# Optimization experiments

Measured on AMD Instinct MI355X. Metric: run time of the kernel, lower is better.

The kernel has to match this reference:

```python
import jax, jax.numpy as jnp
import numpy as np
import math

N_HIDDEN = 256
N_BLOCKS = 15
N_BINARY = 8
NODE_DIM = 16
EDGE_DIM = 4
N_NODES = 20000
N_EDGES = 100000


def setup_inputs() -> dict:
    key = jax.random.key(0)
    ks = iter(jax.random.split(key, 64))

    def lin(i, o):
        return (jax.random.normal(next(ks), (i, o), jnp.float32) / np.sqrt(i)).astype(jnp.float32)

    def lin_s(i, o):  # stacked over N_BLOCKS layers
        return (jax.random.normal(next(ks), (N_BLOCKS, i, o), jnp.float32) / np.sqrt(i)).astype(jnp.float32)

    inp = {
        "x": jax.random.uniform(next(ks), (N_NODES, NODE_DIM), jnp.float32),
        "edge_index": jax.random.randint(next(ks), (2, N_EDGES), 0, N_NODES, jnp.int32),
        "edge_attr": jax.random.uniform(next(ks), (N_EDGES, EDGE_DIM), jnp.float32),
        # conv1: in = NODE_DIM
        "Wq1": lin(NODE_DIM, N_HIDDEN), "bq1": jnp.zeros((N_HIDDEN,), jnp.float32),
        "Wk1": lin(NODE_DIM, N_HIDDEN), "bk1": jnp.zeros((N_HIDDEN,), jnp.float32),
        "Wv1": lin(NODE_DIM, N_HIDDEN), "bv1": jnp.zeros((N_HIDDEN,), jnp.float32),
        "We1": lin(EDGE_DIM, N_HIDDEN),  # lin_edge has no bias in PyG TransformerConv
        "Ws1": lin(NODE_DIM, N_HIDDEN), "bs1": jnp.zeros((N_HIDDEN,), jnp.float32),
        # 15 residual blocks: in = N_HIDDEN, stacked params
        "Wq": lin_s(N_HIDDEN, N_HIDDEN), "bq": jnp.zeros((N_BLOCKS, N_HIDDEN), jnp.float32),
        "Wk": lin_s(N_HIDDEN, N_HIDDEN), "bk": jnp.zeros((N_BLOCKS, N_HIDDEN), jnp.float32),
        "Wv": lin_s(N_HIDDEN, N_HIDDEN), "bv": jnp.zeros((N_BLOCKS, N_HIDDEN), jnp.float32),
        "We": lin_s(EDGE_DIM, N_HIDDEN),
        "Ws": lin_s(N_HIDDEN, N_HIDDEN), "bs": jnp.zeros((N_BLOCKS, N_HIDDEN), jnp.float32),
        # output head
        "Wl": lin(N_HIDDEN, N_BINARY), "bl": jnp.zeros((N_BINARY,), jnp.float32),
        "scale": jnp.asarray([2.0 ** i for i in range(N_BINARY)], jnp.float32),
    }
    return inp


def _tconv(h, ea_emb_src_params, src, dst, n):
    """PyG TransformerConv (heads=1) with edge features."""
    wq, bq, wk, bk, wv, bv, we, ws, bs, ea = ea_emb_src_params
    q = h @ wq + bq          # [N, C]
    k = h @ wk + bk
    v = h @ wv + bv
    e = ea @ we              # [E, C] edge embedding
    ke = k[src] + e          # [E, C]
    alpha = jnp.sum(q[dst] * ke, axis=-1) / math.sqrt(N_HIDDEN)  # [E]
    m = jax.ops.segment_max(alpha, dst, num_segments=n)
    a = jnp.exp(alpha - m[dst])
    s = jax.ops.segment_sum(a, dst, num_segments=n)
    attn = a / (s[dst] + 1e-16)
    out = jax.ops.segment_sum(attn[:, None] * (v[src] + e), dst, num_segments=n)
    return out + h @ ws + bs  # root_weight skip


def reference(x, edge_index, edge_attr,
              Wq1, bq1, Wk1, bk1, Wv1, bv1, We1, Ws1, bs1,
              Wq, bq, Wk, bk, Wv, bv, We, Ws, bs,
              Wl, bl, scale):
    n = x.shape[0]
    src, dst = edge_index[0], edge_index[1]
    h = jnp.log(x + 1.0)
    ea = jnp.log(edge_attr + 1.0)
    h = _tconv(h, (Wq1, bq1, Wk1, bk1, Wv1, bv1, We1, Ws1, bs1, ea), src, dst, n)

    def block(carry, p):
        wq, bq_, wk, bk_, wv, bv_, we, ws, bs_ = p
        std = jax.lax.stop_gradient(jnp.std(carry, axis=-1, ddof=1, keepdims=True))
        h2 = jax.nn.relu(carry / std)
        y = _tconv(h2, (wq, bq_, wk, bk_, wv, bv_, we, ws, bs_, ea), src, dst, n)
        return carry + y, None

    h, _ = jax.lax.scan(block, h, (Wq, bq, Wk, bk, Wv, bv, We, Ws, bs))
    h = h / math.sqrt(N_BLOCKS)
    h = h @ Wl + bl
    return jnp.sum(h * scale, axis=-1, keepdims=True)
```

## Files before the change

### kernel.cpp

```cpp
#include <hip/hip_runtime.h>
#include <math.h>

typedef short bf16x8 __attribute__((ext_vector_type(8)));
typedef float f32x4 __attribute__((ext_vector_type(4)));
typedef _Float16 h16x8 __attribute__((ext_vector_type(8)));
typedef _Float16 h16x4 __attribute__((ext_vector_type(4)));
typedef _Float16 h16x2 __attribute__((ext_vector_type(2)));

static __device__ __forceinline__ float wred_sum(float v){
  #pragma unroll
  for (int o = 32; o > 0; o >>= 1) v += __shfl_xor(v, o, 64);
  return v;
}

static __device__ __forceinline__ unsigned short f2bf(float x){
  union { float f; unsigned int u; } c; c.f = x;
  unsigned int u = c.u;
  return (unsigned short)((u + 0x7FFFu + ((u >> 16) & 1u)) >> 16);
}

__global__ void prep_kernel(const float* __restrict__ x, const float* __restrict__ ea_in,
                            float* __restrict__ hx, float* __restrict__ ea,
                            int nx, int ne){
  int i = blockIdx.x * 256 + threadIdx.x;
  if (i < nx) hx[i] = logf(x[i] + 1.f);
  if (i < ne) ea[i] = logf(ea_in[i] + 1.f);
}

__global__ void zero_kernel(int* __restrict__ c, int n){
  int i = blockIdx.x * 256 + threadIdx.x;
  if (i < n) c[i] = 0;
}

__global__ void hist_kernel(const int* __restrict__ dst, int* __restrict__ counts, int E){
  int i = blockIdx.x * 256 + threadIdx.x;
  if (i < E) atomicAdd(&counts[dst[i]], 1);
}

__global__ __launch_bounds__(1024) void scan_kernel(const int* __restrict__ counts,
                                                    int* __restrict__ row_ptr,
                                                    int* __restrict__ cursor, int N){
  __shared__ int woff[16];
  __shared__ int carry_s;
  int t = threadIdx.x, lane = t & 63, wid = t >> 6;
  if (t == 0) carry_s = 0;
  __syncthreads();
  for (int base = 0; base < N; base += 1024){
    int i = base + t;
    int v = (i < N) ? counts[i] : 0;
    int incl = v;
    #pragma unroll
    for (int o = 1; o < 64; o <<= 1){
      int tmp = __shfl_up(incl, o, 64);
      if (lane >= o) incl += tmp;
    }
    if (lane == 63) woff[wid] = incl;
    __syncthreads();
    if (t < 16){
      int w = woff[t];
      int inc2 = w;
      #pragma unroll
      for (int o = 1; o < 16; o <<= 1){
        int tmp = __shfl_up(inc2, o, 16);
        if (t >= o) inc2 += tmp;
      }
      woff[t] = inc2 - w;
    }
    __syncthreads();
    int ex = carry_s + woff[wid] + incl - v;
    if (i < N){ row_ptr[i] = ex; cursor[i] = ex; }
    __syncthreads();
    if (t == 1023) carry_s = ex + v;
    __syncthreads();
  }
  if (t == 0) row_ptr[N] = carry_s;
}

__global__ void scatter_kernel(const int* __restrict__ src, const int* __restrict__ dst,
                               const float* __restrict__ ea,
                               int* __restrict__ cursor,
                               int* __restrict__ src_csr, float* __restrict__ ea_csr, int E){
  int i = blockIdx.x * 256 + threadIdx.x;
  if (i < E){
    int p = atomicAdd(&cursor[dst[i]], 1);
    src_csr[p] = src[i];
    *(float4*)&ea_csr[(size_t)p * 4] = *(const float4*)&ea[(size_t)i * 4];
  }
}

__global__ void wlscale_kernel(const float* __restrict__ Wl, const float* __restrict__ bl,
                               const float* __restrict__ scale, float* __restrict__ wlsc){
  int c = threadIdx.x;
  float s = 0.f;
  #pragma unroll
  for (int j = 0; j < 8; j++) s += Wl[c * 8 + j] * scale[j];
  wlsc[c] = s;
  if (c == 0){
    float b = 0.f;
    #pragma unroll
    for (int j = 0; j < 8; j++) b += bl[j] * scale[j];
    wlsc[256] = b;
  }
}

__global__ __launch_bounds__(256) void pack_w_kernel(
    const float* __restrict__ Wq, const float* __restrict__ Wk,
    const float* __restrict__ Wv, const float* __restrict__ Ws,
    unsigned short* __restrict__ Wp)
{
  __shared__ float t[32][33];
  int l   = blockIdx.z;
  int k0  = blockIdx.x * 32;
  int n0g = blockIdx.y * 32;
  int w   = n0g >> 8;
  int n0  = n0g & 255;
  const float* W = ((w == 0) ? Wq : (w == 1) ? Wk : (w == 2) ? Wv : Ws) + (size_t)l * 65536;
  int rr = threadIdx.x >> 3;
  int cc = (threadIdx.x & 7) * 4;
  float4 vv = *(const float4*)&W[(size_t)(k0 + rr) * 256 + n0 + cc];
  t[rr][cc + 0] = vv.x; t[rr][cc + 1] = vv.y; t[rr][cc + 2] = vv.z; t[rr][cc + 3] = vv.w;
  __syncthreads();
  ushort4 o;
  o.x = f2bf(t[cc + 0][rr]);
  o.y = f2bf(t[cc + 1][rr]);
  o.z = f2bf(t[cc + 2][rr]);
  o.w = f2bf(t[cc + 3][rr]);
  *(ushort4*)&Wp[(size_t)l * 262144 + (size_t)(n0g + rr) * 256 + k0 + cc] = o;
}

__global__ void pack_b_kernel(const float* __restrict__ bq, const float* __restrict__ bk,
                              const float* __restrict__ bv, const float* __restrict__ bs,
                              float* __restrict__ bp){
  int i = blockIdx.x * 256 + threadIdx.x;
  if (i < 15 * 256){
    int l = i >> 8, n = i & 255;
    bp[l * 1024 + 0   + n] = bq[i];
    bp[l * 1024 + 256 + n] = bk[i];
    bp[l * 1024 + 512 + n] = bv[i];
    bp[l * 1024 + 768 + n] = bs[i];
  }
}

__global__ __launch_bounds__(256) void pack_wqe_kernel(
    const float* __restrict__ Wq, const float* __restrict__ We,
    const float* __restrict__ bq, float* __restrict__ Wqe, float* __restrict__ bqe)
{
  __shared__ float We_s[1024];
  int l = blockIdx.x;
  for (int i = threadIdx.x; i < 1024; i += 256) We_s[i] = We[(size_t)l * 1024 + i];
  __syncthreads();
  int k = threadIdx.x;
  const float* wrow = Wq + (size_t)l * 65536 + (size_t)k * 256;
  float s0 = 0.f, s1 = 0.f, s2 = 0.f, s3 = 0.f;
  for (int c = 0; c < 256; c++){
    float wv = wrow[c];
    s0 += wv * We_s[c];
    s1 += wv * We_s[256 + c];
    s2 += wv * We_s[512 + c];
    s3 += wv * We_s[768 + c];
  }
  float4 o; o.x = s0; o.y = s1; o.z = s2; o.w = s3;
  *(float4*)&Wqe[((size_t)l * 256 + k) * 4] = o;
  if (k < 4){
    float b = 0.f;
    for (int c = 0; c < 256; c++) b += bq[l * 256 + c] * We_s[k * 256 + c];
    bqe[l * 4 + k] = b;
  }
}

__global__ __launch_bounds__(256) void qwe1_kernel(const _Float16* __restrict__ qkvh,
                                                   const float* __restrict__ We1,
                                                   float* __restrict__ qwe, int N){
  __shared__ float We_s[1024];
  for (int i = threadIdx.x; i < 1024; i += 256) We_s[i] = We1[i];
  __syncthreads();
  int wid = threadIdx.x >> 6, lane = threadIdx.x & 63;
  int n = blockIdx.x * 4 + wid;
  if (n >= N) return;
  int c0 = lane * 4;
  h16x4 qr = *(const h16x4*)&qkvh[(size_t)n * 768 + c0];
  float q0 = (float)qr[0], q1 = (float)qr[1], q2 = (float)qr[2], q3 = (float)qr[3];
  float4 o;
  #pragma unroll
  for (int j = 0; j < 4; j++){
    float s = q0 * We_s[j * 256 + c0] + q1 * We_s[j * 256 + c0 + 1]
            + q2 * We_s[j * 256 + c0 + 2] + q3 * We_s[j * 256 + c0 + 3];
    s = wred_sum(s);
    if (j == 0) o.x = s; else if (j == 1) o.y = s; else if (j == 2) o.z = s; else o.w = s;
  }
  if (lane == 0) *(float4*)&qwe[(size_t)n * 4] = o;
}

__global__ __launch_bounds__(256) void gemm1_kernel(
    const float* __restrict__ A,
    const float* __restrict__ W0, const float* __restrict__ W1,
    const float* __restrict__ W2, const float* __restrict__ W3,
    const float* __restrict__ B0, const float* __restrict__ B1,
    const float* __restrict__ B2, const float* __restrict__ B3,
    _Float16* __restrict__ qkvh, _Float16* __restrict__ slh, int N)
{
  __shared__ float As[64][16];
  int nb = blockIdx.x * 64;
  {
    int row = nb + (threadIdx.x >> 2);
    int qq = (threadIdx.x & 3) * 4;
    float4 a = make_float4(0.f, 0.f, 0.f, 0.f);
    if (row < N) a = *(const float4*)&A[row * 16 + qq];
    *(float4*)&As[threadIdx.x >> 2][qq] = a;
  }
  __syncthreads();
  int col = threadIdx.x;
  #pragma unroll
  for (int w = 0; w < 4; w++){
    const float* W  = (w == 0) ? W0 : (w == 1) ? W1 : (w == 2) ? W2 : W3;
    const float* Bi = (w == 0) ? B0 : (w == 1) ? B1 : (w == 2) ? B2 : B3;
    float wr[16];
    #pragma unroll
    for (int kk = 0; kk < 16; kk++) wr[kk] = W[kk * 256 + col];
    float bias = Bi[col];
    for (int r = 0; r < 64; r++){
      int row = nb + r;
      if (row >= N) break;
      float acc = bias;
      #pragma unroll
      for (int kk = 0; kk < 16; kk++) acc += As[r][kk] * wr[kk];
      if (w < 3) qkvh[(size_t)row * 768 + w * 256 + col] = (_Float16)acc;
      else       slh[(size_t)row * 256 + col] = (_Float16)acc;
    }
  }
}

__global__ __launch_bounds__(256, 3) void gemm_mfma_kernel(
    const unsigned short* __restrict__ A,
    const unsigned short* __restrict__ Wp,
    const float* __restrict__ bp,
    _Float16* __restrict__ qkvh,
    _Float16* __restrict__ slh,
    int M)
{
  __shared__ unsigned short lds[2 * 128 * 64];
  unsigned short* ldsA = lds;
  unsigned short* ldsB = lds + 128 * 64;
  const int tid  = threadIdx.x;
  const int wave = tid >> 6, lane = tid & 63;
  const int wm = wave >> 1, wn = wave & 1;
  const int rt  = (int)gridDim.x;
  const int lin = (int)blockIdx.x + rt * (int)blockIdx.y;
  const int gt  = (lin & 7) * rt + (lin >> 3);
  const int m0 = (gt >> 3) * 128;
  const int n0 = (gt & 7) * 128;

  f32x4 acc[4][4] = {};

  const int srow  = lane >> 3;
  const int sc16  = lane & 7;
  const int skgrp = sc16 ^ (srow & 7);

  for (int k0 = 0; k0 < 256; k0 += 64){
    #pragma unroll
    for (int it = 0; it < 4; ++it){
      int lrow = wave * 32 + it * 8;
      const unsigned short* gA = A + (size_t)(m0 + lrow + srow) * 256 + k0 + skgrp * 8;
      __builtin_amdgcn_global_load_lds((const __attribute__((address_space(1))) unsigned int*)gA,
          (__attribute__((address_space(3))) unsigned int*)(ldsA + lrow * 64), 16, 0, 0);
      const unsigned short* gB = Wp + (size_t)(n0 + lrow + srow) * 256 + k0 + skgrp * 8;
      __builtin_amdgcn_global_load_lds((const __attribute__((address_space(1))) unsigned int*)gB,
          (__attribute__((address_space(3))) unsigned int*)(ldsB + lrow * 64), 16, 0, 0);
    }
    __syncthreads();

    bf16x8 af[4][2], bfr[4][2];
    #pragma unroll
    for (int mb = 0; mb < 4; ++mb){
      int r = wm * 64 + mb * 16 + (lane & 15);
      #pragma unroll
      for (int ks = 0; ks < 2; ++ks){
        int kg = ks * 4 + (lane >> 4);
        af[mb][ks] = *(const bf16x8*)&ldsA[r * 64 + ((kg ^ (r & 7)) * 8)];
      }
    }
    #pragma unroll
    for (int nb = 0; nb < 4; ++nb){
      int r = wn * 64 + nb * 16 + (lane & 15);
      #pragma unroll
      for (int ks = 0; ks < 2; ++ks){
        int kg = ks * 4 + (lane >> 4);
        bfr[nb][ks] = *(const bf16x8*)&ldsB[r * 64 + ((kg ^ (r & 7)) * 8)];
      }
    }
    #pragma unroll
    for (int mb = 0; mb < 4; ++mb){
      #pragma unroll
      for (int nb = 0; nb < 4; ++nb){
        acc[mb][nb] = __builtin_amdgcn_mfma_f32_16x16x32_bf16(af[mb][0], bfr[nb][0], acc[mb][nb], 0, 0, 0);
        acc[mb][nb] = __builtin_amdgcn_mfma_f32_16x16x32_bf16(af[mb][1], bfr[nb][1], acc[mb][nb], 0, 0, 0);
      }
    }
    __syncthreads();
  }

  _Float16* lt = (_Float16*)lds;
  #pragma unroll
  for (int nb = 0; nb < 4; ++nb){
    int col = wn * 64 + nb * 16 + (lane & 15);
    float bias = bp[n0 + col];
    #pragma unroll
    for (int mb = 0; mb < 4; ++mb){
      #pragma unroll
      for (int r4 = 0; r4 < 4; ++r4){
        int row = wm * 64 + mb * 16 + (lane >> 4) * 4 + r4;
        lt[row * 128 + (col ^ (((row >> 2) & 3) << 4))] = (_Float16)(acc[mb][nb][r4] + bias);
      }
    }
  }
  __syncthreads();
  int tr = tid >> 4;
  int tc = (tid & 15) * 8;
  if (n0 < 768){
    #pragma unroll
    for (int it = 0; it < 8; ++it){
      int row = tr + it * 16;
      int grow = m0 + row;
      if (grow < M){
        h16x8 v8 = *(const h16x8*)&lt[row * 128 + (tc ^ (((row >> 2) & 3) << 4))];
        *(h16x8*)&qkvh[(size_t)grow * 768 + n0 + tc] = v8;
      }
    }
  } else {
    #pragma unroll
    for (int it = 0; it < 8; ++it){
      int row = tr + it * 16;
      int grow = m0 + row;
      if (grow < M){
        h16x8 v8 = *(const h16x8*)&lt[row * 128 + (tc ^ (((row >> 2) & 3) << 4))];
        *(h16x8*)&slh[(size_t)grow * 256 + (n0 - 768) + tc] = v8;
      }
    }
  }
}

__global__ __launch_bounds__(256) void agg_kernel(
    const _Float16* __restrict__ qkvh,
    const _Float16* __restrict__ slh,
    const float* __restrict__ qwe,
    const float* __restrict__ ea_csr,
    const int* __restrict__ src_csr,
    const float* __restrict__ We,
    const float* __restrict__ Wqe_next,
    const float* __restrict__ bqe_next,
    const int* __restrict__ row_ptr,
    const float* __restrict__ h_in, float* __restrict__ h_out,
    unsigned short* __restrict__ h2b, float* __restrict__ qwe_out,
    const float* __restrict__ wlsc, float* __restrict__ out,
    int RESID, int LAST, int N)
{
  int wid = threadIdx.x >> 6, lane = threadIdx.x & 63;
  int c0 = lane * 4;
  int glane = lane >> 3;
  int slane = lane & 7;
  union hu { h16x8 v; h16x2 p[4]; };
  int stride = (int)gridDim.x * 4;

  for (int n = blockIdx.x * 4 + wid; n < N; n += stride){
    int e0 = row_ptr[n], e1 = row_ptr[n + 1];
    float4 qwe4 = *(const float4*)&qwe[(size_t)n * 4];
    h16x4 slv4 = *(const h16x4*)&slh[(size_t)n * 256 + c0];
    float4 hp = make_float4(0.f, 0.f, 0.f, 0.f);
    if (RESID) hp = *(const float4*)&h_in[(size_t)n * 256 + c0];
    const _Float16* qrow = qkvh + (size_t)n * 768 + slane * 32;
    hu qf[4];
    #pragma unroll
    for (int u = 0; u < 4; ++u) qf[u].v = *(const h16x8*)(qrow + u * 8);

    float m = -INFINITY, ssum = 0.f;
    float a0 = 0.f, a1 = 0.f, a2 = 0.f, a3 = 0.f;
    float ec0 = 0.f, ec1 = 0.f, ec2 = 0.f, ec3 = 0.f;

    for (int base = e0; base < e1; base += 8){
      int cnt = min(8, e1 - base);
      int eg = base + ((glane < cnt) ? glane : (cnt - 1));
      int sg = src_csr[eg];
      int sj[8];
      #pragma unroll
      for (int j = 0; j < 8; ++j) sj[j] = __shfl(sg, j << 3, 64);
      float4 eag = *(const float4*)&ea_csr[(size_t)eg * 4];
      const _Float16* krow = qkvh + (size_t)sg * 768 + 256 + slane * 32;
      float dot = 0.f;
      #pragma unroll
      for (int u = 0; u < 4; ++u){
        hu kf;
        kf.v = *(const h16x8*)(krow + u * 8);
        #pragma unroll
        for (int pp = 0; pp < 4; ++pp){
#if __has_builtin(__builtin_amdgcn_fdot2)
          dot = __builtin_amdgcn_fdot2(qf[u].p[pp], kf.p[pp], dot, false);
#else
          dot += (float)qf[u].p[pp][0] * (float)kf.p[pp][0] + (float)qf[u].p[pp][1] * (float)kf.p[pp][1];
#endif
        }
      }
      #pragma unroll
      for (int o = 1; o < 8; o <<= 1) dot += __shfl_xor(dot, o, 64);
      float alpha_g = (dot + qwe4.x * eag.x + qwe4.y * eag.y + qwe4.z * eag.z + qwe4.w * eag.w) * 0.0625f;
      float aj[8];
      #pragma unroll
      for (int j = 0; j < 8; ++j){
        aj[j] = __shfl(alpha_g, j << 3, 64);
        if (j >= cnt) aj[j] = -INFINITY;
      }
      float mc = fmaxf(fmaxf(fmaxf(aj[0], aj[1]), fmaxf(aj[2], aj[3])),
                       fmaxf(fmaxf(aj[4], aj[5]), fmaxf(aj[6], aj[7])));
      float mn = fmaxf(m, mc);
      float corr = expf(m - mn);
      float wj[8];
      float wtot = 0.f;
      #pragma unroll
      for (int j = 0; j < 8; ++j){
        wj[j] = (j < cnt) ? expf(aj[j] - mn) : 0.f;
        wtot += wj[j];
      }
      ssum = ssum * corr + wtot;
      a0 *= corr; a1 *= corr; a2 *= corr; a3 *= corr;
      ec0 *= corr; ec1 *= corr; ec2 *= corr; ec3 *= corr;
      m = mn;
      #pragma unroll
      for (int j = 0; j < 8; ++j){
        if (j < cnt){
          h16x4 vr = *(const h16x4*)&qkvh[(size_t)sj[j] * 768 + 512 + c0];
          float4 er = *(const float4*)&ea_csr[(size_t)(base + j) * 4];
          a0 += wj[j] * (float)vr[0];
          a1 += wj[j] * (float)vr[1];
          a2 += wj[j] * (float)vr[2];
          a3 += wj[j] * (float)vr[3];
          ec0 += wj[j] * er.x;
          ec1 += wj[j] * er.y;
          ec2 += wj[j] * er.z;
          ec3 += wj[j] * er.w;
        }
      }
    }

    float inv = 1.f / (ssum + 1e-16f);
    float4 W0 = *(const float4*)&We[0 * 256 + c0];
    float4 W1 = *(const float4*)&We[1 * 256 + c0];
    float4 W2 = *(const float4*)&We[2 * 256 + c0];
    float4 W3 = *(const float4*)&We[3 * 256 + c0];
    float emb0 = ec0 * W0.x + ec1 * W1.x + ec2 * W2.x + ec3 * W3.x;
    float emb1 = ec0 * W0.y + ec1 * W1.y + ec2 * W2.y + ec3 * W3.y;
    float emb2 = ec0 * W0.z + ec1 * W1.z + ec2 * W2.z + ec3 * W3.z;
    float emb3 = ec0 * W0.w + ec1 * W1.w + ec2 * W2.w + ec3 * W3.w;
    float y0 = (a0 + emb0) * inv + (float)slv4[0];
    float y1 = (a1 + emb1) * inv + (float)slv4[1];
    float y2 = (a2 + emb2) * inv + (float)slv4[2];
    float y3 = (a3 + emb3) * inv + (float)slv4[3];
    float o0 = hp.x + y0, o1 = hp.y + y1, o2 = hp.z + y2, o3 = hp.w + y3;
    if (LAST){
      float4 wv = *(const float4*)&wlsc[c0];
      float pp = o0 * wv.x + o1 * wv.y + o2 * wv.z + o3 * wv.w;
      pp = wred_sum(pp);
      if (lane == 0) out[n] = pp * (1.f / sqrtf(15.f)) + wlsc[256];
      continue;
    }
    float4 ho; ho.x = o0; ho.y = o1; ho.z = o2; ho.w = o3;
    *(float4*)&h_out[(size_t)n * 256 + c0] = ho;
    float mean = wred_sum(o0 + o1 + o2 + o3) * (1.f / 256.f);
    float d0 = o0 - mean, d1 = o1 - mean, d2 = o2 - mean, d3 = o3 - mean;
    float var = wred_sum(d0 * d0 + d1 * d1 + d2 * d2 + d3 * d3) * (1.f / 255.f);
    float invstd = 1.f / sqrtf(var);
    float t0 = fmaxf(o0 * invstd, 0.f);
    float t1 = fmaxf(o1 * invstd, 0.f);
    float t2 = fmaxf(o2 * invstd, 0.f);
    float t3 = fmaxf(o3 * invstd, 0.f);
    ushort4 hb;
    hb.x = f2bf(t0); hb.y = f2bf(t1); hb.z = f2bf(t2); hb.w = f2bf(t3);
    *(ushort4*)&h2b[(size_t)n * 256 + c0] = hb;
    if (Wqe_next){
      float4 g0 = *(const float4*)&Wqe_next[(c0 + 0) * 4];
      float4 g1 = *(const float4*)&Wqe_next[(c0 + 1) * 4];
      float4 g2 = *(const float4*)&Wqe_next[(c0 + 2) * 4];
      float4 g3 = *(const float4*)&Wqe_next[(c0 + 3) * 4];
      float s0 = t0 * g0.x + t1 * g1.x + t2 * g2.x + t3 * g3.x;
      float s1 = t0 * g0.y + t1 * g1.y + t2 * g2.y + t3 * g3.y;
      float s2 = t0 * g0.z + t1 * g1.z + t2 * g2.z + t3 * g3.z;
      float s3 = t0 * g0.w + t1 * g1.w + t2 * g2.w + t3 * g3.w;
      s0 = wred_sum(s0); s1 = wred_sum(s1); s2 = wred_sum(s2); s3 = wred_sum(s3);
      if (lane == 0){
        float4 bq4 = *(const float4*)bqe_next;
        float4 o; o.x = s0 + bq4.x; o.y = s1 + bq4.y; o.z = s2 + bq4.z; o.w = s3 + bq4.w;
        *(float4*)&qwe_out[(size_t)n * 4] = o;
      }
    }
  }
}

extern "C" void kernel_launch(void* const* d_in, const int* in_sizes, int n_in,
                              void* d_out, int out_size, void* d_ws, size_t ws_size,
                              hipStream_t stream)
{
  const float* x     = (const float*)d_in[0];
  const int*   eidx  = (const int*)d_in[1];
  const float* Wq1 = (const float*)d_in[3];  const float* bq1 = (const float*)d_in[4];
  const float* Wk1 = (const float*)d_in[5];  const float* bk1 = (const float*)d_in[6];
  const float* Wv1 = (const float*)d_in[7];  const float* bv1 = (const float*)d_in[8];
  const float* We1 = (const float*)d_in[9];
  const float* Ws1 = (const float*)d_in[10]; const float* bs1 = (const float*)d_in[11];
  const float* Wq = (const float*)d_in[12];  const float* bq = (const float*)d_in[13];
  const float* Wk = (const float*)d_in[14];  const float* bk = (const float*)d_in[15];
  const float* Wv = (const float*)d_in[16];  const float* bv = (const float*)d_in[17];
  const float* We = (const float*)d_in[18];
  const float* Ws = (const float*)d_in[19];  const float* bs = (const float*)d_in[20];
  const float* Wl = (const float*)d_in[21];  const float* bl = (const float*)d_in[22];
  const float* scale = (const float*)d_in[23];
  (void)n_in; (void)ws_size;

  int N = in_sizes[0] / 16;
  int E = in_sizes[2] / 4;
  int Mpad = (N + 127) & ~127;
  float* out = (float*)d_out;
  (void)out_size;

  char* p = (char*)d_ws;
  auto alloc = [&](size_t bytes) -> char* {
    char* r = p; p += (bytes + 255) & ~(size_t)255; return r;
  };
  float* hx   = (float*)alloc((size_t)N * 16 * 4);
  float* ea   = (float*)alloc((size_t)E * 4 * 4);
  float* h    = (float*)alloc((size_t)N * 256 * 4);
  unsigned short* h2b = (unsigned short*)alloc((size_t)Mpad * 256 * 2);
  _Float16* qkvh = (_Float16*)alloc((size_t)N * 768 * 2);
  _Float16* slh  = (_Float16*)alloc((size_t)N * 256 * 2);
  float* qwe  = (float*)alloc((size_t)N * 4 * 4);
  float* ea_csr = (float*)alloc((size_t)E * 4 * 4);
  int* src_csr  = (int*)alloc((size_t)E * 4);
  unsigned short* Wp  = (unsigned short*)alloc((size_t)15 * 1024 * 256 * 2);
  float* bp   = (float*)alloc((size_t)15 * 1024 * 4);
  float* Wqe  = (float*)alloc((size_t)15 * 256 * 4 * 4);
  float* bqe  = (float*)alloc((size_t)15 * 4 * 4);
  float* wlsc = (float*)alloc(257 * 4);
  int* counts  = (int*)alloc((size_t)N * 4);
  int* cursor  = (int*)alloc((size_t)N * 4);
  int* row_ptr = (int*)alloc(((size_t)N + 1) * 4);

  const int* srcp = eidx;
  const int* dstp = eidx + E;

  int nx = N * 16, ne = E * 4;
  int big = nx > ne ? nx : ne;

  zero_kernel<<<(N + 255) / 256, 256, 0, stream>>>(counts, N);
  prep_kernel<<<(big + 255) / 256, 256, 0, stream>>>(x, (const float*)d_in[2], hx, ea, nx, ne);
  hist_kernel<<<(E + 255) / 256, 256, 0, stream>>>(dstp, counts, E);
  scan_kernel<<<1, 1024, 0, stream>>>(counts, row_ptr, cursor, N);
  scatter_kernel<<<(E + 255) / 256, 256, 0, stream>>>(srcp, dstp, ea, cursor,
                                                      src_csr, ea_csr, E);
  wlscale_kernel<<<1, 256, 0, stream>>>(Wl, bl, scale, wlsc);
  pack_w_kernel<<<dim3(8, 32, 15), 256, 0, stream>>>(Wq, Wk, Wv, Ws, Wp);
  pack_b_kernel<<<15, 256, 0, stream>>>(bq, bk, bv, bs, bp);
  pack_wqe_kernel<<<15, 256, 0, stream>>>(Wq, We, bq, Wqe, bqe);

  int agg_blocks = 1280;

  gemm1_kernel<<<(N + 63) / 64, 256, 0, stream>>>(hx, Wq1, Wk1, Wv1, Ws1,
                                                  bq1, bk1, bv1, bs1, qkvh, slh, N);
  qwe1_kernel<<<(N + 3) / 4, 256, 0, stream>>>(qkvh, We1, qwe, N);
  agg_kernel<<<agg_blocks, 256, 0, stream>>>(qkvh, slh, qwe, ea_csr, src_csr, We1,
                                             Wqe, bqe, row_ptr,
                                             h, h, h2b, qwe, wlsc, out, 0, 0, N);

  for (int l = 0; l < 15; l++){
    gemm_mfma_kernel<<<dim3(Mpad / 128, 8), 256, 0, stream>>>(
        h2b, Wp + (size_t)l * 262144, bp + (size_t)l * 1024, qkvh, slh, N);
    int last = (l == 14);
    const float* wqe_n = (l < 14) ? (Wqe + (size_t)(l + 1) * 1024) : nullptr;
    const float* bqe_n = (l < 14) ? (bqe + (size_t)(l + 1) * 4) : nullptr;
    agg_kernel<<<agg_blocks, 256, 0, stream>>>(qkvh, slh, qwe, ea_csr, src_csr,
                                               We + (size_t)l * 1024,
                                               wqe_n, bqe_n, row_ptr,
                                               h, h, h2b, qwe, wlsc, out, 1, last, N);
  }
}
```

Baseline: 1.165 ms.

## Process two nodes per wavefront in aggregation and store residual in fp16

The aggregation kernel now assigns one node per half-wavefront (32 lanes, 8 channels each) instead of one node per full wavefront, and launches one block per 8 nodes instead of a grid-stride loop. The residual state h is stored as fp16 instead of fp32, which halves its read and write traffic. This aims to raise memory-level parallelism and cut bytes moved in the gather-heavy aggregation. The cost is lane divergence when the two nodes in a wavefront have different degrees, since both halves run the larger trip count. The fp16 residual accumulated over 15 blocks also loses precision.

```diff
diff --git a/kernel.cpp b/kernel.cpp
--- a/kernel.cpp
+++ b/kernel.cpp
@@ -10,6 +10,12 @@
 static __device__ __forceinline__ float wred_sum(float v){
   #pragma unroll
   for (int o = 32; o > 0; o >>= 1) v += __shfl_xor(v, o, 64);
+  return v;
+}
+
+static __device__ __forceinline__ float hred_sum(float v){
+  #pragma unroll
+  for (int o = 16; o > 0; o >>= 1) v += __shfl_xor(v, o, 64);
   return v;
 }
 
@@ -349,146 +355,169 @@
     const float* __restrict__ Wqe_next,
     const float* __restrict__ bqe_next,
     const int* __restrict__ row_ptr,
-    const float* __restrict__ h_in, float* __restrict__ h_out,
+    const _Float16* __restrict__ h_in, _Float16* __restrict__ h_out,
     unsigned short* __restrict__ h2b, float* __restrict__ qwe_out,
     const float* __restrict__ wlsc, float* __restrict__ out,
-    int RESID, int LAST, int N)
+    int RESID, int LAST, int N, int E)
 {
   int wid = threadIdx.x >> 6, lane = threadIdx.x & 63;
-  int c0 = lane * 4;
-  int glane = lane >> 3;
-  int slane = lane & 7;
+  int half = lane >> 5, hl = lane & 31;
+  int n = blockIdx.x * 8 + wid * 2 + half;
+  bool valid = (n < N);
+  int nn = valid ? n : (N - 1);
+  int c0 = hl * 8;
+  int glane = hl >> 2;
+  int slane = hl & 3;
   union hu { h16x8 v; h16x2 p[4]; };
-  int stride = (int)gridDim.x * 4;
-
-  for (int n = blockIdx.x * 4 + wid; n < N; n += stride){
-    int e0 = row_ptr[n], e1 = row_ptr[n + 1];
-    float4 qwe4 = *(const float4*)&qwe[(size_t)n * 4];
-    h16x4 slv4 = *(const h16x4*)&slh[(size_t)n * 256 + c0];
-    float4 hp = make_float4(0.f, 0.f, 0.f, 0.f);
-    if (RESID) hp = *(const float4*)&h_in[(size_t)n * 256 + c0];
-    const _Float16* qrow = qkvh + (size_t)n * 768 + slane * 32;
-    hu qf[4];
-    #pragma unroll
-    for (int u = 0; u < 4; ++u) qf[u].v = *(const h16x8*)(qrow + u * 8);
-
-    float m = -INFINITY, ssum = 0.f;
-    float a0 = 0.f, a1 = 0.f, a2 = 0.f, a3 = 0.f;
-    float ec0 = 0.f, ec1 = 0.f, ec2 = 0.f, ec3 = 0.f;
-
-    for (int base = e0; base < e1; base += 8){
-      int cnt = min(8, e1 - base);
-      int eg = base + ((glane < cnt) ? glane : (cnt - 1));
-      int sg = src_csr[eg];
-      int sj[8];
+
+  int e0 = row_ptr[nn], e1 = row_ptr[nn + 1];
+  float4 qwe4 = *(const float4*)&qwe[(size_t)nn * 4];
+  h16x8 slv = *(const h16x8*)&slh[(size_t)nn * 256 + c0];
+  h16x8 hpv = {};
+  if (RESID) hpv = *(const h16x8*)&h_in[(size_t)nn * 256 + c0];
+  const _Float16* qrow = qkvh + (size_t)nn * 768 + slane * 64;
+  hu qf[8];
+  #pragma unroll
+  for (int u = 0; u < 8; ++u) qf[u].v = *(const h16x8*)(qrow + u * 8);
+
+  float m = -INFINITY, ssum = 0.f;
+  float a[8] = {};
+  float ec[4] = {};
+
+  int nch = (e1 - e0 + 7) >> 3;
+  int nco = __shfl_xor(nch, 32, 64);
+  int ntrip = nch > nco ? nch : nco;
+
+  for (int it = 0; it < ntrip; ++it){
+    int base = e0 + it * 8;
+    int cnt = e1 - base; if (cnt > 8) cnt = 8;
+    int off = (cnt > 0) ? ((glane < cnt) ? glane : cnt - 1) : 0;
+    int eg = base + off;
+    if (eg >= E) eg = E - 1;
+    int sg = src_csr[eg];
+    int sj[8];
+    #pragma unroll
+    for (int j = 0; j < 8; ++j) sj[j] = __shfl(sg, (half << 5) + (j << 2), 64);
+    float4 eag = *(const float4*)&ea_csr[(size_t)eg * 4];
+    const _Float16* krow = qkvh + (size_t)sg * 768 + 256 + slane * 64;
+    float dot = 0.f;
+    #pragma unroll
+    for (int u = 0; u < 8; ++u){
+      hu kf;
+      kf.v = *(const h16x8*)(krow + u * 8);
       #pragma unroll
-      for (int j = 0; j < 8; ++j) sj[j] = __shfl(sg, j << 3, 64);
-      float4 eag = *(const float4*)&ea_csr[(size_t)eg * 4];
-      const _Float16* krow = qkvh + (size_t)sg * 768 + 256 + slane * 32;
-      float dot = 0.f;
-      #pragma unroll
-      for (int u = 0; u < 4; ++u){
-        hu kf;
-        kf.v = *(const h16x8*)(krow + u * 8);
+      for (int pp = 0; pp < 4; ++pp){
+#if __has_builtin(__builtin_amdgcn_fdot2)
+        dot = __builtin_amdgcn_fdot2(qf[u].p[pp], kf.p[pp], dot, false);
+#else
+        dot += (float)qf[u].p[pp][0] * (float)kf.p[pp][0] + (float)qf[u].p[pp][1] * (float)kf.p[pp][1];
+#endif
+      }
+    }
+    dot += __shfl_xor(dot, 1, 64);
+    dot += __shfl_xor(dot, 2, 64);
+    float alpha_g = (dot + qwe4.x * eag.x + qwe4.y * eag.y + qwe4.z * eag.z + qwe4.w * eag.w) * 0.0625f;
+    float aj[8];
+    #pragma unroll
+    for (int j = 0; j < 8; ++j){
+      aj[j] = __shfl(alpha_g, (half << 5) + (j << 2), 64);
+      if (j >= cnt) aj[j] = -INFINITY;
+    }
+    float mc = fmaxf(fmaxf(fmaxf(aj[0], aj[1]), fmaxf(aj[2], aj[3])),
+                     fmaxf(fmaxf(aj[4], aj[5]), fmaxf(aj[6], aj[7])));
+    float mn = fmaxf(m, mc);
+    float corr = (mn > -INFINITY) ? expf(m - mn) : 0.f;
+    float wj[8];
+    float wtot = 0.f;
+    #pragma unroll
+    for (int j = 0; j < 8; ++j){
+      wj[j] = (j < cnt) ? expf(aj[j] - mn) : 0.f;
+      wtot += wj[j];
+    }
+    ssum = ssum * corr + wtot;
+    #pragma unroll
+    for (int i = 0; i < 8; ++i) a[i] *= corr;
+    #pragma unroll
+    for (int i = 0; i < 4; ++i) ec[i] *= corr;
+    m = mn;
+    #pragma unroll
+    for (int j = 0; j < 8; ++j){
+      if (j < cnt){
+        h16x8 vr = *(const h16x8*)&qkvh[(size_t)sj[j] * 768 + 512 + c0];
+        float4 er = *(const float4*)&ea_csr[(size_t)(base + j) * 4];
         #pragma unroll
-        for (int pp = 0; pp < 4; ++pp){
-#if __has_builtin(__builtin_amdgcn_fdot2)
-          dot = __builtin_amdgcn_fdot2(qf[u].p[pp], kf.p[pp], dot, false);
-#else
-          dot += (float)qf[u].p[pp][0] * (float)kf.p[pp][0] + (float)qf[u].p[pp][1] * (float)kf.p[pp][1];
-#endif
-        }
-      }
-      #pragma unroll
-      for (int o = 1; o < 8; o <<= 1) dot += __shfl_xor(dot, o, 64);
-      float alpha_g = (dot + qwe4.x * eag.x + qwe4.y * eag.y + qwe4.z * eag.z + qwe4.w * eag.w) * 0.0625f;
-      float aj[8];
-      #pragma unroll
-      for (int j = 0; j < 8; ++j){
-        aj[j] = __shfl(alpha_g, j << 3, 64);
-        if (j >= cnt) aj[j] = -INFINITY;
-      }
-      float mc = fmaxf(fmaxf(fmaxf(aj[0], aj[1]), fmaxf(aj[2], aj[3])),
-                       fmaxf(fmaxf(aj[4], aj[5]), fmaxf(aj[6], aj[7])));
-      float mn = fmaxf(m, mc);
-      float corr = expf(m - mn);
-      float wj[8];
-      float wtot = 0.f;
-      #pragma unroll
-      for (int j = 0; j < 8; ++j){
-        wj[j] = (j < cnt) ? expf(aj[j] - mn) : 0.f;
-        wtot += wj[j];
-      }
-      ssum = ssum * corr + wtot;
-      a0 *= corr; a1 *= corr; a2 *= corr; a3 *= corr;
-      ec0 *= corr; ec1 *= corr; ec2 *= corr; ec3 *= corr;
-      m = mn;
-      #pragma unroll
-      for (int j = 0; j < 8; ++j){
-        if (j < cnt){
-          h16x4 vr = *(const h16x4*)&qkvh[(size_t)sj[j] * 768 + 512 + c0];
-          float4 er = *(const float4*)&ea_csr[(size_t)(base + j) * 4];
-          a0 += wj[j] * (float)vr[0];
-          a1 += wj[j] * (float)vr[1];
-          a2 += wj[j] * (float)vr[2];
-          a3 += wj[j] * (float)vr[3];
-          ec0 += wj[j] * er.x;
-          ec1 += wj[j] * er.y;
-          ec2 += wj[j] * er.z;
-          ec3 += wj[j] * er.w;
-        }
-      }
-    }
-
-    float inv = 1.f / (ssum + 1e-16f);
-    float4 W0 = *(const float4*)&We[0 * 256 + c0];
-    float4 W1 = *(const float4*)&We[1 * 256 + c0];
-    float4 W2 = *(const float4*)&We[2 * 256 + c0];
-    float4 W3 = *(const float4*)&We[3 * 256 + c0];
-    float emb0 = ec0 * W0.x + ec1 * W1.x + ec2 * W2.x + ec3 * W3.x;
-    float emb1 = ec0 * W0.y + ec1 * W1.y + ec2 * W2.y + ec3 * W3.y;
-    float emb2 = ec0 * W0.z + ec1 * W1.z + ec2 * W2.z + ec3 * W3.z;
-    float emb3 = ec0 * W0.w + ec1 * W1.w + ec2 * W2.w + ec3 * W3.w;
-    float y0 = (a0 + emb0) * inv + (float)slv4[0];
-    float y1 = (a1 + emb1) * inv + (float)slv4[1];
-    float y2 = (a2 + emb2) * inv + (float)slv4[2];
-    float y3 = (a3 + emb3) * inv + (float)slv4[3];
-    float o0 = hp.x + y0, o1 = hp.y + y1, o2 = hp.z + y2, o3 = hp.w + y3;
-    if (LAST){
-      float4 wv = *(const float4*)&wlsc[c0];
-      float pp = o0 * wv.x + o1 * wv.y + o2 * wv.z + o3 * wv.w;
-      pp = wred_sum(pp);
-      if (lane == 0) out[n] = pp * (1.f / sqrtf(15.f)) + wlsc[256];
-      continue;
-    }
-    float4 ho; ho.x = o0; ho.y = o1; ho.z = o2; ho.w = o3;
-    *(float4*)&h_out[(size_t)n * 256 + c0] = ho;
-    float mean = wred_sum(o0 + o1 + o2 + o3) * (1.f / 256.f);
-    float d0 = o0 - mean, d1 = o1 - mean, d2 = o2 - mean, d3 = o3 - mean;
-    float var = wred_sum(d0 * d0 + d1 * d1 + d2 * d2 + d3 * d3) * (1.f / 255.f);
-    float invstd = 1.f / sqrtf(var);
-    float t0 = fmaxf(o0 * invstd, 0.f);
-    float t1 = fmaxf(o1 * invstd, 0.f);
-    float t2 = fmaxf(o2 * invstd, 0.f);
-    float t3 = fmaxf(o3 * invstd, 0.f);
-    ushort4 hb;
-    hb.x = f2bf(t0); hb.y = f2bf(t1); hb.z = f2bf(t2); hb.w = f2bf(t3);
-    *(ushort4*)&h2b[(size_t)n * 256 + c0] = hb;
-    if (Wqe_next){
-      float4 g0 = *(const float4*)&Wqe_next[(c0 + 0) * 4];
-      float4 g1 = *(const float4*)&Wqe_next[(c0 + 1) * 4];
-      float4 g2 = *(const float4*)&Wqe_next[(c0 + 2) * 4];
-      float4 g3 = *(const float4*)&Wqe_next[(c0 + 3) * 4];
-      float s0 = t0 * g0.x + t1 * g1.x + t2 * g2.x + t3 * g3.x;
-      float s1 = t0 * g0.y + t1 * g1.y + t2 * g2.y + t3 * g3.y;
-      float s2 = t0 * g0.z + t1 * g1.z + t2 * g2.z + t3 * g3.z;
-      float s3 = t0 * g0.w + t1 * g1.w + t2 * g2.w + t3 * g3.w;
-      s0 = wred_sum(s0); s1 = wred_sum(s1); s2 = wred_sum(s2); s3 = wred_sum(s3);
-      if (lane == 0){
-        float4 bq4 = *(const float4*)bqe_next;
-        float4 o; o.x = s0 + bq4.x; o.y = s1 + bq4.y; o.z = s2 + bq4.z; o.w = s3 + bq4.w;
-        *(float4*)&qwe_out[(size_t)n * 4] = o;
-      }
+        for (int i = 0; i < 8; ++i) a[i] += wj[j] * (float)vr[i];
+        ec[0] += wj[j] * er.x;
+        ec[1] += wj[j] * er.y;
+        ec[2] += wj[j] * er.z;
+        ec[3] += wj[j] * er.w;
+      }
+    }
+  }
+
+  float inv = 1.f / (ssum + 1e-16f);
+  float o[8];
+  #pragma unroll
+  for (int g = 0; g < 2; ++g){
+    float4 w0 = *(const float4*)&We[0 * 256 + c0 + g * 4];
+    float4 w1 = *(const float4*)&We[1 * 256 + c0 + g * 4];
+    float4 w2 = *(const float4*)&We[2 * 256 + c0 + g * 4];
+    float4 w3 = *(const float4*)&We[3 * 256 + c0 + g * 4];
+    float e0v = ec[0] * w0.x + ec[1] * w1.x + ec[2] * w2.x + ec[3] * w3.x;
+    float e1v = ec[0] * w0.y + ec[1] * w1.y + ec[2] * w2.y + ec[3] * w3.y;
+    float e2v = ec[0] * w0.z + ec[1] * w1.z + ec[2] * w2.z + ec[3] * w3.z;
+    float e3v = ec[0] * w0.w + ec[1] * w1.w + ec[2] * w2.w + ec[3] * w3.w;
+    o[g * 4 + 0] = (a[g * 4 + 0] + e0v) * inv + (float)slv[g * 4 + 0] + (RESID ? (float)hpv[g * 4 + 0] : 0.f);
+    o[g * 4 + 1] = (a[g * 4 + 1] + e1v) * inv + (float)slv[g * 4 + 1] + (RESID ? (float)hpv[g * 4 + 1] : 0.f);
+    o[g * 4 + 2] = (a[g * 4 + 2] + e2v) * inv + (float)slv[g * 4 + 2] + (RESID ? (float)hpv[g * 4 + 2] : 0.f);
+    o[g * 4 + 3] = (a[g * 4 + 3] + e3v) * inv + (float)slv[g * 4 + 3] + (RESID ? (float)hpv[g * 4 + 3] : 0.f);
+  }
+
+  if (LAST){
+    float pp = 0.f;
+    #pragma unroll
+    for (int i = 0; i < 8; ++i) pp += o[i] * wlsc[c0 + i];
+    pp = hred_sum(pp);
+    if (hl == 0 && valid) out[n] = pp * (1.f / sqrtf(15.f)) + wlsc[256];
+    return;
+  }
+
+  if (valid){
+    h16x8 ho;
+    #pragma unroll
+    for (int i = 0; i < 8; ++i) ho[i] = (_Float16)o[i];
+    *(h16x8*)&h_out[(size_t)n * 256 + c0] = ho;
+  }
+  float s = 0.f;
+  #pragma unroll
+  for (int i = 0; i < 8; ++i) s += o[i];
+  float mean = hred_sum(s) * (1.f / 256.f);
+  float vv = 0.f;
+  #pragma unroll
+  for (int i = 0; i < 8; ++i){ float d = o[i] - mean; vv += d * d; }
+  float var = hred_sum(vv) * (1.f / 255.f);
+  float invstd = 1.f / sqrtf(var);
+  float t[8];
+  #pragma unroll
+  for (int i = 0; i < 8; ++i) t[i] = fmaxf(o[i] * invstd, 0.f);
+  if (valid){
+    bf16x8 hb;
+    #pragma unroll
+    for (int i = 0; i < 8; ++i) hb[i] = (short)f2bf(t[i]);
+    *(bf16x8*)&h2b[(size_t)n * 256 + c0] = hb;
+  }
+  if (Wqe_next){
+    float s0 = 0.f, s1 = 0.f, s2 = 0.f, s3 = 0.f;
+    #pragma unroll
+    for (int i = 0; i < 8; ++i){
+      float4 g = *(const float4*)&Wqe_next[(c0 + i) * 4];
+      s0 += t[i] * g.x; s1 += t[i] * g.y; s2 += t[i] * g.z; s3 += t[i] * g.w;
+    }
+    s0 = hred_sum(s0); s1 = hred_sum(s1); s2 = hred_sum(s2); s3 = hred_sum(s3);
+    if (hl == 0 && valid){
+      float4 bq4 = *(const float4*)bqe_next;
+      float4 ov; ov.x = s0 + bq4.x; ov.y = s1 + bq4.y; ov.z = s2 + bq4.z; ov.w = s3 + bq4.w;
+      *(float4*)&qwe_out[(size_t)n * 4] = ov;
     }
   }
 }
@@ -525,7 +554,7 @@
   };
   float* hx   = (float*)alloc((size_t)N * 16 * 4);
   float* ea   = (float*)alloc((size_t)E * 4 * 4);
-  float* h    = (float*)alloc((size_t)N * 256 * 4);
+  _Float16* hh = (_Float16*)alloc((size_t)N * 256 * 2);
   unsigned short* h2b = (unsigned short*)alloc((size_t)Mpad * 256 * 2);
   _Float16* qkvh = (_Float16*)alloc((size_t)N * 768 * 2);
   _Float16* slh  = (_Float16*)alloc((size_t)N * 256 * 2);
@@ -558,14 +587,14 @@
   pack_b_kernel<<<15, 256, 0, stream>>>(bq, bk, bv, bs, bp);
   pack_wqe_kernel<<<15, 256, 0, stream>>>(Wq, We, bq, Wqe, bqe);
 
-  int agg_blocks = 1280;
+  int agg_blocks = (N + 7) / 8;
 
   gemm1_kernel<<<(N + 63) / 64, 256, 0, stream>>>(hx, Wq1, Wk1, Wv1, Ws1,
                                                   bq1, bk1, bv1, bs1, qkvh, slh, N);
   qwe1_kernel<<<(N + 3) / 4, 256, 0, stream>>>(qkvh, We1, qwe, N);
   agg_kernel<<<agg_blocks, 256, 0, stream>>>(qkvh, slh, qwe, ea_csr, src_csr, We1,
                                              Wqe, bqe, row_ptr,
-                                             h, h, h2b, qwe, wlsc, out, 0, 0, N);
+                                             hh, hh, h2b, qwe, wlsc, out, 0, 0, N, E);
 
   for (int l = 0; l < 15; l++){
     gemm_mfma_kernel<<<dim3(Mpad / 128, 8), 256, 0, stream>>>(
@@ -576,6 +605,6 @@
     agg_kernel<<<agg_blocks, 256, 0, stream>>>(qkvh, slh, qwe, ea_csr, src_csr,
                                                We + (size_t)l * 1024,
                                                wqe_n, bqe_n, row_ptr,
-                                               h, h, h2b, qwe, wlsc, out, 1, last, N);
-  }
-}
+                                               hh, hh, h2b, qwe, wlsc, out, 1, last, N, E);
+  }
+}
```

After: 1.155 ms. No clear change (-0.8%).

## Store residual stream in fp16 and launch one wave per node in aggregation

Applied to the files above, without the earlier changes.

The residual hidden state h moves from fp32 to fp16, halving its read and write traffic in every aggregation pass. The grid-stride loop is replaced by one wavefront per node with a grid sized to N/4 blocks. Source-index broadcasts are now done on demand inside the value-gather loop rather than precomputed into an array, which lowers register pressure. The cost is accumulating the residual over 15 blocks in fp16, which may lose accuracy.

```diff
diff --git a/kernel.cpp b/kernel.cpp
--- a/kernel.cpp
+++ b/kernel.cpp
@@ -349,146 +349,148 @@
     const float* __restrict__ Wqe_next,
     const float* __restrict__ bqe_next,
     const int* __restrict__ row_ptr,
-    const float* __restrict__ h_in, float* __restrict__ h_out,
+    const _Float16* __restrict__ h_in, _Float16* __restrict__ h_out,
     unsigned short* __restrict__ h2b, float* __restrict__ qwe_out,
     const float* __restrict__ wlsc, float* __restrict__ out,
     int RESID, int LAST, int N)
 {
   int wid = threadIdx.x >> 6, lane = threadIdx.x & 63;
+  int n = blockIdx.x * 4 + wid;
+  if (n >= N) return;
   int c0 = lane * 4;
   int glane = lane >> 3;
   int slane = lane & 7;
   union hu { h16x8 v; h16x2 p[4]; };
-  int stride = (int)gridDim.x * 4;
-
-  for (int n = blockIdx.x * 4 + wid; n < N; n += stride){
-    int e0 = row_ptr[n], e1 = row_ptr[n + 1];
-    float4 qwe4 = *(const float4*)&qwe[(size_t)n * 4];
-    h16x4 slv4 = *(const h16x4*)&slh[(size_t)n * 256 + c0];
-    float4 hp = make_float4(0.f, 0.f, 0.f, 0.f);
-    if (RESID) hp = *(const float4*)&h_in[(size_t)n * 256 + c0];
-    const _Float16* qrow = qkvh + (size_t)n * 768 + slane * 32;
-    hu qf[4];
-    #pragma unroll
-    for (int u = 0; u < 4; ++u) qf[u].v = *(const h16x8*)(qrow + u * 8);
-
-    float m = -INFINITY, ssum = 0.f;
-    float a0 = 0.f, a1 = 0.f, a2 = 0.f, a3 = 0.f;
-    float ec0 = 0.f, ec1 = 0.f, ec2 = 0.f, ec3 = 0.f;
-
-    for (int base = e0; base < e1; base += 8){
-      int cnt = min(8, e1 - base);
-      int eg = base + ((glane < cnt) ? glane : (cnt - 1));
-      int sg = src_csr[eg];
-      int sj[8];
-      #pragma unroll
-      for (int j = 0; j < 8; ++j) sj[j] = __shfl(sg, j << 3, 64);
-      float4 eag = *(const float4*)&ea_csr[(size_t)eg * 4];
-      const _Float16* krow = qkvh + (size_t)sg * 768 + 256 + slane * 32;
-      float dot = 0.f;
-      #pragma unroll
-      for (int u = 0; u < 4; ++u){
-        hu kf;
-        kf.v = *(const h16x8*)(krow + u * 8);
-        #pragma unroll
-        for (int pp = 0; pp < 4; ++pp){
+
+  int e0 = row_ptr[n], e1 = row_ptr[n + 1];
+  float4 qwe4 = *(const float4*)&qwe[(size_t)n * 4];
+  h16x4 slv4 = *(const h16x4*)&slh[(size_t)n * 256 + c0];
+  h16x4 hpv = {};
+  if (RESID) hpv = *(const h16x4*)&h_in[(size_t)n * 256 + c0];
+  const _Float16* qrow = qkvh + (size_t)n * 768 + slane * 32;
+  hu qf[4];
+  #pragma unroll
+  for (int u = 0; u < 4; ++u) qf[u].v = *(const h16x8*)(qrow + u * 8);
+
+  float m = -INFINITY, ssum = 0.f;
+  float a0 = 0.f, a1 = 0.f, a2 = 0.f, a3 = 0.f;
+  float ec0 = 0.f, ec1 = 0.f, ec2 = 0.f, ec3 = 0.f;
+
+  for (int base = e0; base < e1; base += 8){
+    int cnt = min(8, e1 - base);
+    int eg = base + ((glane < cnt) ? glane : (cnt - 1));
+    int sg = src_csr[eg];
+    float4 eag = *(const float4*)&ea_csr[(size_t)eg * 4];
+    const _Float16* krow = qkvh + (size_t)sg * 768 + 256 + slane * 32;
+    float dot = 0.f;
+    #pragma unroll
+    for (int u = 0; u < 4; ++u){
+      hu kf;
+      kf.v = *(const h16x8*)(krow + u * 8);
+      #pragma unroll
+      for (int pp = 0; pp < 4; ++pp){
 #if __has_builtin(__builtin_amdgcn_fdot2)
-          dot = __builtin_amdgcn_fdot2(qf[u].p[pp], kf.p[pp], dot, false);
+        dot = __builtin_amdgcn_fdot2(qf[u].p[pp], kf.p[pp], dot, false);
 #else
-          dot += (float)qf[u].p[pp][0] * (float)kf.p[pp][0] + (float)qf[u].p[pp][1] * (float)kf.p[pp][1];
+        dot += (float)qf[u].p[pp][0] * (float)kf.p[pp][0] + (float)qf[u].p[pp][1] * (float)kf.p[pp][1];
 #endif
-        }
-      }
-      #pragma unroll
-      for (int o = 1; o < 8; o <<= 1) dot += __shfl_xor(dot, o, 64);
-      float alpha_g = (dot + qwe4.x * eag.x + qwe4.y * eag.y + qwe4.z * eag.z + qwe4.w * eag.w) * 0.0625f;
-      float aj[8];
-      #pragma unroll
-      for (int j = 0; j < 8; ++j){
-        aj[j] = __shfl(alpha_g, j << 3, 64);
-        if (j >= cnt) aj[j] = -INFINITY;
-      }
-      float mc = fmaxf(fmaxf(fmaxf(aj[0], aj[1]), fmaxf(aj[2], aj[3])),
-                       fmaxf(fmaxf(aj[4], aj[5]), fmaxf(aj[6], aj[7])));
-      float mn = fmaxf(m, mc);
-      float corr = expf(m - mn);
-      float wj[8];
-      float wtot = 0.f;
-      #pragma unroll
-      for (int j = 0; j < 8; ++j){
-        wj[j] = (j < cnt) ? expf(aj[j] - mn) : 0.f;
-        wtot += wj[j];
-      }
-      ssum = ssum * corr + wtot;
-      a0 *= corr; a1 *= corr; a2 *= corr; a3 *= corr;
-      ec0 *= corr; ec1 *= corr; ec2 *= corr; ec3 *= corr;
-      m = mn;
-      #pragma unroll
-      for (int j = 0; j < 8; ++j){
-        if (j < cnt){
-          h16x4 vr = *(const h16x4*)&qkvh[(size_t)sj[j] * 768 + 512 + c0];
-          float4 er = *(const float4*)&ea_csr[(size_t)(base + j) * 4];
-          a0 += wj[j] * (float)vr[0];
-          a1 += wj[j] * (float)vr[1];
-          a2 += wj[j] * (float)vr[2];
-          a3 += wj[j] * (float)vr[3];
-          ec0 += wj[j] * er.x;
-          ec1 += wj[j] * er.y;
-          ec2 += wj[j] * er.z;
-          ec3 += wj[j] * er.w;
-        }
-      }
-    }
-
-    float inv = 1.f / (ssum + 1e-16f);
-    float4 W0 = *(const float4*)&We[0 * 256 + c0];
-    float4 W1 = *(const float4*)&We[1 * 256 + c0];
-    float4 W2 = *(const float4*)&We[2 * 256 + c0];
-    float4 W3 = *(const float4*)&We[3 * 256 + c0];
-    float emb0 = ec0 * W0.x + ec1 * W1.x + ec2 * W2.x + ec3 * W3.x;
-    float emb1 = ec0 * W0.y + ec1 * W1.y + ec2 * W2.y + ec3 * W3.y;
-    float emb2 = ec0 * W0.z + ec1 * W1.z + ec2 * W2.z + ec3 * W3.z;
-    float emb3 = ec0 * W0.w + ec1 * W1.w + ec2 * W2.w + ec3 * W3.w;
-    float y0 = (a0 + emb0) * inv + (float)slv4[0];
-    float y1 = (a1 + emb1) * inv + (float)slv4[1];
-    float y2 = (a2 + emb2) * inv + (float)slv4[2];
-    float y3 = (a3 + emb3) * inv + (float)slv4[3];
-    float o0 = hp.x + y0, o1 = hp.y + y1, o2 = hp.z + y2, o3 = hp.w + y3;
-    if (LAST){
-      float4 wv = *(const float4*)&wlsc[c0];
-      float pp = o0 * wv.x + o1 * wv.y + o2 * wv.z + o3 * wv.w;
-      pp = wred_sum(pp);
-      if (lane == 0) out[n] = pp * (1.f / sqrtf(15.f)) + wlsc[256];
-      continue;
-    }
-    float4 ho; ho.x = o0; ho.y = o1; ho.z = o2; ho.w = o3;
-    *(float4*)&h_out[(size_t)n * 256 + c0] = ho;
-    float mean = wred_sum(o0 + o1 + o2 + o3) * (1.f / 256.f);
-    float d0 = o0 - mean, d1 = o1 - mean, d2 = o2 - mean, d3 = o3 - mean;
-    float var = wred_sum(d0 * d0 + d1 * d1 + d2 * d2 + d3 * d3) * (1.f / 255.f);
-    float invstd = 1.f / sqrtf(var);
-    float t0 = fmaxf(o0 * invstd, 0.f);
-    float t1 = fmaxf(o1 * invstd, 0.f);
-    float t2 = fmaxf(o2 * invstd, 0.f);
-    float t3 = fmaxf(o3 * invstd, 0.f);
-    ushort4 hb;
-    hb.x = f2bf(t0); hb.y = f2bf(t1); hb.z = f2bf(t2); hb.w = f2bf(t3);
-    *(ushort4*)&h2b[(size_t)n * 256 + c0] = hb;
-    if (Wqe_next){
-      float4 g0 = *(const float4*)&Wqe_next[(c0 + 0) * 4];
-      float4 g1 = *(const float4*)&Wqe_next[(c0 + 1) * 4];
-      float4 g2 = *(const float4*)&Wqe_next[(c0 + 2) * 4];
-      float4 g3 = *(const float4*)&Wqe_next[(c0 + 3) * 4];
-      float s0 = t0 * g0.x + t1 * g1.x + t2 * g2.x + t3 * g3.x;
-      float s1 = t0 * g0.y + t1 * g1.y + t2 * g2.y + t3 * g3.y;
-      float s2 = t0 * g0.z + t1 * g1.z + t2 * g2.z + t3 * g3.z;
-      float s3 = t0 * g0.w + t1 * g1.w + t2 * g2.w + t3 * g3.w;
-      s0 = wred_sum(s0); s1 = wred_sum(s1); s2 = wred_sum(s2); s3 = wred_sum(s3);
-      if (lane == 0){
-        float4 bq4 = *(const float4*)bqe_next;
-        float4 o; o.x = s0 + bq4.x; o.y = s1 + bq4.y; o.z = s2 + bq4.z; o.w = s3 + bq4.w;
-        *(float4*)&qwe_out[(size_t)n * 4] = o;
-      }
+      }
+    }
+    #pragma unroll
+    for (int o = 1; o < 8; o <<= 1) dot += __shfl_xor(dot, o, 64);
+    float alpha_g = (dot + qwe4.x * eag.x + qwe4.y * eag.y + qwe4.z * eag.z + qwe4.w * eag.w) * 0.0625f;
+    float aj[8];
+    #pragma unroll
+    for (int j = 0; j < 8; ++j){
+      aj[j] = __shfl(alpha_g, j << 3, 64);
+      if (j >= cnt) aj[j] = -INFINITY;
+    }
+    float mc = fmaxf(fmaxf(fmaxf(aj[0], aj[1]), fmaxf(aj[2], aj[3])),
+                     fmaxf(fmaxf(aj[4], aj[5]), fmaxf(aj[6], aj[7])));
+    float mn = fmaxf(m, mc);
+    float corr = expf(m - mn);
+    float wj[8];
+    float wtot = 0.f;
+    #pragma unroll
+    for (int j = 0; j < 8; ++j){
+      wj[j] = (j < cnt) ? expf(aj[j] - mn) : 0.f;
+      wtot += wj[j];
+    }
+    ssum = ssum * corr + wtot;
+    a0 *= corr; a1 *= corr; a2 *= corr; a3 *= corr;
+    ec0 *= corr; ec1 *= corr; ec2 *= corr; ec3 *= corr;
+    m = mn;
+    int sg_bc = sg;
+    #pragma unroll
+    for (int j = 0; j < 8; ++j){
+      if (j < cnt){
+        int sj = __shfl(sg_bc, j << 3, 64);
+        h16x4 vr = *(const h16x4*)&qkvh[(size_t)sj * 768 + 512 + c0];
+        float4 er = *(const float4*)&ea_csr[(size_t)(base + j) * 4];
+        a0 += wj[j] * (float)vr[0];
+        a1 += wj[j] * (float)vr[1];
+        a2 += wj[j] * (float)vr[2];
+        a3 += wj[j] * (float)vr[3];
+        ec0 += wj[j] * er.x;
+        ec1 += wj[j] * er.y;
+        ec2 += wj[j] * er.z;
+        ec3 += wj[j] * er.w;
+      }
+    }
+  }
+
+  float inv = 1.f / (ssum + 1e-16f);
+  float4 W0 = *(const float4*)&We[0 * 256 + c0];
+  float4 W1 = *(const float4*)&We[1 * 256 + c0];
+  float4 W2 = *(const float4*)&We[2 * 256 + c0];
+  float4 W3 = *(const float4*)&We[3 * 256 + c0];
+  float emb0 = ec0 * W0.x + ec1 * W1.x + ec2 * W2.x + ec3 * W3.x;
+  float emb1 = ec0 * W0.y + ec1 * W1.y + ec2 * W2.y + ec3 * W3.y;
+  float emb2 = ec0 * W0.z + ec1 * W1.z + ec2 * W2.z + ec3 * W3.z;
+  float emb3 = ec0 * W0.w + ec1 * W1.w + ec2 * W2.w + ec3 * W3.w;
+  float y0 = (a0 + emb0) * inv + (float)slv4[0];
+  float y1 = (a1 + emb1) * inv + (float)slv4[1];
+  float y2 = (a2 + emb2) * inv + (float)slv4[2];
+  float y3 = (a3 + emb3) * inv + (float)slv4[3];
+  float o0 = y0, o1 = y1, o2 = y2, o3 = y3;
+  if (RESID){
+    o0 += (float)hpv[0]; o1 += (float)hpv[1]; o2 += (float)hpv[2]; o3 += (float)hpv[3];
+  }
+  if (LAST){
+    float4 wv = *(const float4*)&wlsc[c0];
+    float pp = o0 * wv.x + o1 * wv.y + o2 * wv.z + o3 * wv.w;
+    pp = wred_sum(pp);
+    if (lane == 0) out[n] = pp * (1.f / sqrtf(15.f)) + wlsc[256];
+    return;
+  }
+  h16x4 ho;
+  ho[0] = (_Float16)o0; ho[1] = (_Float16)o1; ho[2] = (_Float16)o2; ho[3] = (_Float16)o3;
+  *(h16x4*)&h_out[(size_t)n * 256 + c0] = ho;
+  float mean = wred_sum(o0 + o1 + o2 + o3) * (1.f / 256.f);
+  float d0 = o0 - mean, d1 = o1 - mean, d2 = o2 - mean, d3 = o3 - mean;
+  float var = wred_sum(d0 * d0 + d1 * d1 + d2 * d2 + d3 * d3) * (1.f / 255.f);
+  float invstd = 1.f / sqrtf(var);
+  float t0 = fmaxf(o0 * invstd, 0.f);
+  float t1 = fmaxf(o1 * invstd, 0.f);
+  float t2 = fmaxf(o2 * invstd, 0.f);
+  float t3 = fmaxf(o3 * invstd, 0.f);
+  ushort4 hb;
+  hb.x = f2bf(t0); hb.y = f2bf(t1); hb.z = f2bf(t2); hb.w = f2bf(t3);
+  *(ushort4*)&h2b[(size_t)n * 256 + c0] = hb;
+  if (Wqe_next){
+    float4 g0 = *(const float4*)&Wqe_next[(c0 + 0) * 4];
+    float4 g1 = *(const float4*)&Wqe_next[(c0 + 1) * 4];
+    float4 g2 = *(const float4*)&Wqe_next[(c0 + 2) * 4];
+    float4 g3 = *(const float4*)&Wqe_next[(c0 + 3) * 4];
+    float s0 = t0 * g0.x + t1 * g1.x + t2 * g2.x + t3 * g3.x;
+    float s1 = t0 * g0.y + t1 * g1.y + t2 * g2.y + t3 * g3.y;
+    float s2 = t0 * g0.z + t1 * g1.z + t2 * g2.z + t3 * g3.z;
+    float s3 = t0 * g0.w + t1 * g1.w + t2 * g2.w + t3 * g3.w;
+    s0 = wred_sum(s0); s1 = wred_sum(s1); s2 = wred_sum(s2); s3 = wred_sum(s3);
+    if (lane == 0){
+      float4 bq4 = *(const float4*)bqe_next;
+      float4 o; o.x = s0 + bq4.x; o.y = s1 + bq4.y; o.z = s2 + bq4.z; o.w = s3 + bq4.w;
+      *(float4*)&qwe_out[(size_t)n * 4] = o;
     }
   }
 }
@@ -525,7 +527,7 @@
   };
   float* hx   = (float*)alloc((size_t)N * 16 * 4);
   float* ea   = (float*)alloc((size_t)E * 4 * 4);
-  float* h    = (float*)alloc((size_t)N * 256 * 4);
+  _Float16* hh = (_Float16*)alloc((size_t)N * 256 * 2);
   unsigned short* h2b = (unsigned short*)alloc((size_t)Mpad * 256 * 2);
   _Float16* qkvh = (_Float16*)alloc((size_t)N * 768 * 2);
   _Float16* slh  = (_Float16*)alloc((size_t)N * 256 * 2);
@@ -558,14 +560,14 @@
   pack_b_kernel<<<15, 256, 0, stream>>>(bq, bk, bv, bs, bp);
   pack_wqe_kernel<<<15, 256, 0, stream>>>(Wq, We, bq, Wqe, bqe);
 
-  int agg_blocks = 1280;
+  int agg_blocks = (N + 3) / 4;
 
   gemm1_kernel<<<(N + 63) / 64, 256, 0, stream>>>(hx, Wq1, Wk1, Wv1, Ws1,
                                                   bq1, bk1, bv1, bs1, qkvh, slh, N);
   qwe1_kernel<<<(N + 3) / 4, 256, 0, stream>>>(qkvh, We1, qwe, N);
   agg_kernel<<<agg_blocks, 256, 0, stream>>>(qkvh, slh, qwe, ea_csr, src_csr, We1,
                                              Wqe, bqe, row_ptr,
-                                             h, h, h2b, qwe, wlsc, out, 0, 0, N);
+                                             hh, hh, h2b, qwe, wlsc, out, 0, 0, N);
 
   for (int l = 0; l < 15; l++){
     gemm_mfma_kernel<<<dim3(Mpad / 128, 8), 256, 0, stream>>>(
@@ -576,6 +578,6 @@
     agg_kernel<<<agg_blocks, 256, 0, stream>>>(qkvh, slh, qwe, ea_csr, src_csr,
                                                We + (size_t)l * 1024,
                                                wqe_n, bqe_n, row_ptr,
-                                               h, h, h2b, qwe, wlsc, out, 1, last, N);
-  }
-}
+                                               hh, hh, h2b, qwe, wlsc, out, 1, last, N);
+  }
+}
```

Measured after the change: 1.075 ms. -7.7%, faster.
